# Optimization experiments

Measured on AMD Instinct MI355X. Metric: run time of the kernel, lower is better.

The kernel has to match this reference:

```python
import jax, jax.numpy as jnp
import numpy as np

NUM_HEADS = 12


def setup_inputs() -> dict:
    key = jax.random.key(0)
    ks = jax.random.split(key, 10)
    B, N, C = 8, 1024, 768
    H = NUM_HEADS
    return {
        "x": jax.random.normal(ks[0], (B, N, C), dtype=jnp.float32),
        "geometric": jax.random.uniform(ks[1], (B, 1, 1, 1), dtype=jnp.float32),
        "text": jax.random.uniform(ks[2], (B, 1, 1, 1), dtype=jnp.float32),
        "color": jax.random.uniform(ks[3], (B, 1, 1, 1), dtype=jnp.float32),
        "W_qkv": jax.random.normal(ks[4], (C, 3 * C), dtype=jnp.float32) * 0.02,
        "W_proj": jax.random.normal(ks[5], (C, C), dtype=jnp.float32) * 0.02,
        "b_proj": jax.random.normal(ks[6], (C,), dtype=jnp.float32) * 0.02,
        "geo_bias": jax.random.normal(ks[7], (1, H, 1, 1), dtype=jnp.float32) * 0.1,
        "txt_bias": jax.random.normal(ks[8], (1, H, 1, 1), dtype=jnp.float32) * 0.1,
        "col_bias": jax.random.normal(ks[9], (1, H, 1, 1), dtype=jnp.float32) * 0.1,
    }


def reference(x, geometric, text, color, W_qkv, W_proj, b_proj, geo_bias, txt_bias, col_bias):
    B, N, C = x.shape
    H = NUM_HEADS
    Dh = C // H
    scale = Dh ** -0.5
    # qkv: [B, N, 3, H, Dh] -> q,k,v each [B, H, N, Dh]
    qkv = (x @ W_qkv).reshape(B, N, 3, H, Dh)
    q = jnp.transpose(qkv[:, :, 0], (0, 2, 1, 3))
    k = jnp.transpose(qkv[:, :, 1], (0, 2, 1, 3))
    v = jnp.transpose(qkv[:, :, 2], (0, 2, 1, 3))
    # scores [B, H, N, N] with additive per-head logo biases
    attn = jnp.einsum("bhnd,bhmd->bhnm", q, k) * scale
    attn = attn + geo_bias * geometric + txt_bias * text + col_bias * color
    attn = jax.nn.softmax(attn, axis=-1)
    out = jnp.einsum("bhnm,bhmd->bhnd", attn, v)  # [B, H, N, Dh]
    out = jnp.transpose(out, (0, 2, 1, 3)).reshape(B, N, C)
    return out @ W_proj + b_proj
```

## Files before the change

kernel.cpp:

```cpp
#include <hip/hip_runtime.h>
#include <hip/hip_bf16.h>


typedef __bf16 b16x8 __attribute__((ext_vector_type(8)));
typedef float f32x4 __attribute__((ext_vector_type(4)));

__device__ __forceinline__ ushort f2b(float f) {
    union { float f; uint u; } v; v.f = f;
    uint u = v.u;
    u += 0x7fffu + ((u >> 16) & 1u);
    return (ushort)(u >> 16);
}

__device__ __forceinline__ uint packbf(float a, float b) {
    union { float f; uint u; } ua, ub; ua.f = a; ub.f = b;
    return ((ua.u + 0x8000u) >> 16) | ((ub.u + 0x8000u) & 0xffff0000u);
}

__device__ __forceinline__ void async_cp16(const void* g, void* l) {
    __builtin_amdgcn_global_load_lds(
        (const __attribute__((address_space(1))) unsigned int*)g,
        (__attribute__((address_space(3))) unsigned int*)l, 16, 0, 0);
}


__global__ __launch_bounds__(256)
void k_prep(const float* __restrict__ x, ushort* __restrict__ xb,
            const float* __restrict__ Wqkv, ushort* __restrict__ wqkvt,
            const float* __restrict__ Wproj, ushort* __restrict__ wprojt) {
    __shared__ ushort T[64][65];
    const int blk = blockIdx.x;
    const int t   = threadIdx.x;

    if (blk < 6144) {
        const int i = blk * 256 + t;
        const float4 v = reinterpret_cast<const float4*>(x)[i];
        ushort4 o;
        o.x = f2b(v.x); o.y = f2b(v.y); o.z = f2b(v.z); o.w = f2b(v.w);
        reinterpret_cast<ushort4*>(xb)[i] = o;
        return;
    }

    const bool isqkv = (blk < 6576);
    const int idx = isqkv ? (blk - 6144) : (blk - 6576);
    const int Nin = isqkv ? 2304 : 768;
    const float* W  = isqkv ? Wqkv : Wproj;
    ushort* Wt      = isqkv ? wqkvt : wprojt;
    const int k0 = (idx % 12) * 64;
    const int n0 = (idx / 12) * 64;
    const int r  = t >> 4, cg = (t & 15) * 4;
    #pragma unroll
    for (int rr = 0; rr < 64; rr += 16) {
        const float4 v = *reinterpret_cast<const float4*>(&W[(size_t)(k0 + r + rr) * Nin + n0 + cg]);
        T[r + rr][cg + 0] = f2b(v.x); T[r + rr][cg + 1] = f2b(v.y);
        T[r + rr][cg + 2] = f2b(v.z); T[r + rr][cg + 3] = f2b(v.w);
    }
    __syncthreads();
    #pragma unroll
    for (int rr = 0; rr < 64; rr += 16) {
        ushort4 o;
        o.x = T[cg + 0][r + rr]; o.y = T[cg + 1][r + rr];
        o.z = T[cg + 2][r + rr]; o.w = T[cg + 3][r + rr];
        *reinterpret_cast<ushort4*>(&Wt[(size_t)(n0 + r + rr) * 768 + k0 + cg]) = o;
    }
}


#define SBAR()   asm volatile("s_barrier" ::: "memory")
#define WAITV3() asm volatile("s_waitcnt vmcnt(3)" ::: "memory")
#define WAITV0() asm volatile("s_waitcnt vmcnt(0)" ::: "memory")

#define LDSA(buf, kh, ii) (*reinterpret_cast<const b16x8*>( \
    &lds[(buf) * 16384 + (kh) * 8192 + (wm * 64 + (ii) * 16 + m16) * 32 + q8s]))
#define LDSB(buf, kh, jj) (*reinterpret_cast<const b16x8*>( \
    &lds[32768 + (buf) * 8192 + (kh) * 4096 + (wn * 64 + (jj) * 16 + m16) * 32 + q8s]))

#define STA(bufn, ktv, kh) { \
    async_cp16(aA0 + (ktv) + (kh) * 32, &lds[(bufn)*16384 + (kh)*8192 + tid*8]); \
    async_cp16(aA1 + (ktv) + (kh) * 32, &lds[(bufn)*16384 + (kh)*8192 + 4096 + tid*8]); }
#define STB(bufn, ktv, kh) { \
    async_cp16(aB0 + (ktv) + (kh) * 32, &lds[32768 + (bufn)*8192 + (kh)*4096 + tid*8]); }

#define MPAIR(I0, kh, bufc) { \
    const b16x8 a0 = LDSA(bufc, kh, (I0)+0), a1 = LDSA(bufc, kh, (I0)+1); \
    if (vblk) { \
        _Pragma("unroll") \
        for (int j = 0; j < 4; j++) { \
            acc[(I0)+0][j] = __builtin_amdgcn_mfma_f32_16x16x32_bf16(a0, bf[j], acc[(I0)+0][j], 0, 0, 0); \
            acc[(I0)+1][j] = __builtin_amdgcn_mfma_f32_16x16x32_bf16(a1, bf[j], acc[(I0)+1][j], 0, 0, 0); \
        } \
    } else { \
        _Pragma("unroll") \
        for (int j = 0; j < 4; j++) { \
            acc[(I0)+0][j] = __builtin_amdgcn_mfma_f32_16x16x32_bf16(bf[j], a0, acc[(I0)+0][j], 0, 0, 0); \
            acc[(I0)+1][j] = __builtin_amdgcn_mfma_f32_16x16x32_bf16(bf[j], a1, acc[(I0)+1][j], 0, 0, 0); \
        } \
    } }

__global__ __launch_bounds__(512, 1)
void k_qkv(const ushort* __restrict__ A, const ushort* __restrict__ Bt,
           ushort* __restrict__ qo, ushort* __restrict__ ko,
           ushort* __restrict__ vo) {
    extern __shared__ ushort lds[];
    const int id   = blockIdx.x;
    const int xcd  = id & 7;
    const int s    = id >> 3;
    const int by   = xcd * 4 + s / 18;
    const int bx   = s % 18;
    const int tid  = threadIdx.x;
    const int w    = tid >> 6;
    const int lane = tid & 63;
    const int wm   = w >> 1, wn = w & 1;
    const int m16  = lane & 15, quad = lane >> 4;
    const int q8   = quad * 8;
    const int q8s  = q8 ^ ((m16 & 8) ? 16 : 0);
    const int mbase = by * 256, nbase = bx * 128;
    const int colbase = nbase + wn * 64;
    const bool vblk = (nbase >= 1536);
    const int tr   = tid >> 2;
    const int ssub = ((tid & 3) * 8) ^ ((tr & 8) ? 16 : 0);

    const ushort* aA0 = &A [(size_t)(mbase +       tr) * 768 + ssub];
    const ushort* aA1 = &A [(size_t)(mbase + 128 + tr) * 768 + ssub];
    const ushort* aB0 = &Bt[(size_t)(nbase +       tr) * 768 + ssub];

    f32x4 acc[4][4];
    #pragma unroll
    for (int i = 0; i < 4; i++)
        #pragma unroll
        for (int j = 0; j < 4; j++) acc[i][j] = (f32x4){0.f, 0.f, 0.f, 0.f};

    STA(0, 0, 0); STB(0, 0, 0);
    STA(0, 0, 1); STB(0, 0, 1);
    WAITV3();
    SBAR();

    b16x8 bf[4];
    int cur = 0;
    for (int t = 0; t < 12; t++) {
        const int kt  = t * 64;
        const int nxt = cur ^ 1;
        const bool more = (t < 11);
        #pragma unroll
        for (int j = 0; j < 4; j++) bf[j] = LDSB(cur, 0, j);
        if (more) STA(nxt, kt + 64, 0);
        __builtin_amdgcn_s_setprio(1);
        MPAIR(0, 0, cur);
        __builtin_amdgcn_s_setprio(0);
        SBAR();
        if (more) STB(nxt, kt + 64, 0);
        __builtin_amdgcn_s_setprio(1);
        MPAIR(2, 0, cur);
        __builtin_amdgcn_s_setprio(0);
        if (more) { WAITV3(); } else { WAITV0(); }
        SBAR();
        #pragma unroll
        for (int j = 0; j < 4; j++) bf[j] = LDSB(cur, 1, j);
        if (more) STA(nxt, kt + 64, 1);
        __builtin_amdgcn_s_setprio(1);
        MPAIR(0, 1, cur);
        __builtin_amdgcn_s_setprio(0);
        SBAR();
        if (more) STB(nxt, kt + 64, 1);
        __builtin_amdgcn_s_setprio(1);
        MPAIR(2, 1, cur);
        __builtin_amdgcn_s_setprio(0);
        if (more) {
            WAITV3();
            SBAR();
        }
        cur = nxt;
    }

    if (vblk) {
        #pragma unroll
        for (int j = 0; j < 4; j++) {
            const int rem = colbase + j * 16 + m16 - 1536;
            const int h = rem >> 6, d0 = rem & 63;
            #pragma unroll
            for (int i = 0; i < 4; i++) {
                const int tok0 = mbase + wm * 64 + i * 16 + quad * 4;
                const int b = tok0 >> 10, n0 = tok0 & 1023;
                ushort4 pk;
                pk.x = f2b(acc[i][j][0]); pk.y = f2b(acc[i][j][1]);
                pk.z = f2b(acc[i][j][2]); pk.w = f2b(acc[i][j][3]);
                *reinterpret_cast<ushort4*>(
                    &vo[((size_t)(b * 12 + h) * 64 + d0) * 1024 + n0]) = pk;
            }
        }
    } else {
        ushort* base  = (nbase >= 768) ? ko : qo;
        const int off = (nbase >= 768) ? 768 : 0;
        #pragma unroll
        for (int j = 0; j < 4; j++) {
            const int f0 = colbase + j * 16 + quad * 4 - off;
            const int h = f0 >> 6, d0 = f0 & 63;
            #pragma unroll
            for (int i = 0; i < 4; i++) {
                const int tok = mbase + wm * 64 + i * 16 + m16;
                const int b = tok >> 10, n = tok & 1023;
                ushort4 pk;
                pk.x = f2b(acc[i][j][0]); pk.y = f2b(acc[i][j][1]);
                pk.z = f2b(acc[i][j][2]); pk.w = f2b(acc[i][j][3]);
                *reinterpret_cast<ushort4*>(
                    &base[((size_t)(b * 12 + h) * 1024 + n) * 64 + d0]) = pk;
            }
        }
    }
}


__global__ __launch_bounds__(256, 2)
void k_proj(const ushort* __restrict__ A, const ushort* __restrict__ Bt,
            float* __restrict__ co, const float* __restrict__ bias,
            int N, int K) {
    __shared__ ushort As[2][128 * 32];
    __shared__ ushort Bs[2][128 * 32];
    const int id   = blockIdx.x;
    const int xcd  = id & 7;
    const int s    = id >> 3;
    const int by   = xcd * 8 + (s & 7);
    const int bx   = s >> 3;
    const int tid  = threadIdx.x;
    const int lane = tid & 63;
    const int w    = tid >> 6;
    const int wm   = w >> 1, wn = w & 1;
    const int m16  = lane & 15, quad = lane >> 4;
    const int mbase = by * 128, nbase = bx * 128;

    f32x4 acc[4][4];
    #pragma unroll
    for (int i = 0; i < 4; i++)
        #pragma unroll
        for (int j = 0; j < 4; j++) acc[i][j] = (f32x4){0.f, 0.f, 0.f, 0.f};

    const int rS = w * 32 + (lane >> 2);
    const int cS = (lane & 3) * 8;
    const int wOff0 = (w * 2 + 0) * 512;
    const int wOff1 = (w * 2 + 1) * 512;
    const ushort* gA0 = &A [(size_t)(mbase + rS)      * K + cS];
    const ushort* gA1 = &A [(size_t)(mbase + rS + 16) * K + cS];
    const ushort* gB0 = &Bt[(size_t)(nbase + rS)      * K + cS];
    const ushort* gB1 = &Bt[(size_t)(nbase + rS + 16) * K + cS];

    async_cp16(gA0, &As[0][wOff0]);
    async_cp16(gA1, &As[0][wOff1]);
    async_cp16(gB0, &Bs[0][wOff0]);
    async_cp16(gB1, &Bs[0][wOff1]);

    for (int kt = 0; kt < K; kt += 32) {
        const int cur = (kt >> 5) & 1, nxt = cur ^ 1;
        __syncthreads();
        if (kt + 32 < K) {
            async_cp16(gA0 + kt + 32, &As[nxt][wOff0]);
            async_cp16(gA1 + kt + 32, &As[nxt][wOff1]);
            async_cp16(gB0 + kt + 32, &Bs[nxt][wOff0]);
            async_cp16(gB1 + kt + 32, &Bs[nxt][wOff1]);
        }
        b16x8 af[4], bfr[4];
        #pragma unroll
        for (int i = 0; i < 4; i++)
            af[i] = *reinterpret_cast<const b16x8*>(&As[cur][(wm * 64 + i * 16 + m16) * 32 + quad * 8]);
        #pragma unroll
        for (int j = 0; j < 4; j++)
            bfr[j] = *reinterpret_cast<const b16x8*>(&Bs[cur][(wn * 64 + j * 16 + m16) * 32 + quad * 8]);
        #pragma unroll
        for (int i = 0; i < 4; i++)
            #pragma unroll
            for (int j = 0; j < 4; j++)
                acc[i][j] = __builtin_amdgcn_mfma_f32_16x16x32_bf16(bfr[j], af[i], acc[i][j], 0, 0, 0);
    }

    #pragma unroll
    for (int j = 0; j < 4; j++) {
        const int f0 = nbase + wn * 64 + j * 16 + quad * 4;
        #pragma unroll
        for (int i = 0; i < 4; i++) {
            const int tok = mbase + wm * 64 + i * 16 + m16;
            float4 val;
            val.x = acc[i][j][0] + bias[f0 + 0];
            val.y = acc[i][j][1] + bias[f0 + 1];
            val.z = acc[i][j][2] + bias[f0 + 2];
            val.w = acc[i][j][3] + bias[f0 + 3];
            *reinterpret_cast<float4*>(&co[(size_t)tok * N + f0]) = val;
        }
    }
}


#define AP 72

__global__ __launch_bounds__(256)
void k_attn(const ushort* __restrict__ qa, const ushort* __restrict__ ka,
            const ushort* __restrict__ vt, ushort* __restrict__ ao) {
    __shared__ ushort Ks[64 * AP];
    __shared__ ushort Vs[64 * AP];

    const int l    = blockIdx.x;
    const int xcd  = l & 7;
    const int g    = l >> 3;
    const int head = (g % 12) * 8 + xcd;
    const int qsup = g / 12;
    const int tid  = threadIdx.x;
    const int w    = tid >> 6;
    const int lane = tid & 63;
    const int n    = lane & 15;
    const int q    = lane >> 4;

    const ushort* qh = qa + (size_t)head * 65536;
    const ushort* kh = ka + (size_t)head * 65536;
    const ushort* vh = vt + (size_t)head * 65536;
    const int qrow0 = qsup * 128 + w * 32;

    b16x8 bq0[2], bq1[2];
    #pragma unroll
    for (int u = 0; u < 2; u++) {
        bq0[u] = *reinterpret_cast<const b16x8*>(&qh[(qrow0 + u * 16 + n) * 64 + q * 8]);
        bq1[u] = *reinterpret_cast<const b16x8*>(&qh[(qrow0 + u * 16 + n) * 64 + 32 + q * 8]);
    }

    const int kr0 = tid >> 3, kc0 = (tid & 7) * 8;
    const int kr1 = kr0 + 32, kc1 = kc0;

    int4 kg0, kg1, vg0, vg1;
    kg0 = *reinterpret_cast<const int4*>(&kh[(0 + kr0) * 64 + kc0]);
    kg1 = *reinterpret_cast<const int4*>(&kh[(0 + kr1) * 64 + kc1]);
    vg0 = *reinterpret_cast<const int4*>(&vh[kr0 * 1024 + 0 + kc0]);
    vg1 = *reinterpret_cast<const int4*>(&vh[kr1 * 1024 + 0 + kc1]);

    f32x4 o[2][4];
    #pragma unroll
    for (int u = 0; u < 2; u++)
        #pragma unroll
        for (int dt = 0; dt < 4; dt++) o[u][dt] = (f32x4){0, 0, 0, 0};
    float Lacc[2] = {0.f, 0.f};

    const float SC = 0.125f * 1.4426950408889634f;
    const int s0 = ((q & 1) * 2) * 16 + n;
    const int s1 = s0 + 16;
    const bool lowq = (q < 2);

    for (int m0 = 0; m0 < 1024; m0 += 64) {
        *reinterpret_cast<int4*>(&Ks[kr0 * AP + kc0]) = kg0;
        *reinterpret_cast<int4*>(&Ks[kr1 * AP + kc1]) = kg1;
        *reinterpret_cast<int4*>(&Vs[kr0 * AP + kc0]) = vg0;
        *reinterpret_cast<int4*>(&Vs[kr1 * AP + kc1]) = vg1;
        __syncthreads();

        if (m0 + 64 < 1024) {
            kg0 = *reinterpret_cast<const int4*>(&kh[(m0 + 64 + kr0) * 64 + kc0]);
            kg1 = *reinterpret_cast<const int4*>(&kh[(m0 + 64 + kr1) * 64 + kc1]);
            vg0 = *reinterpret_cast<const int4*>(&vh[kr0 * 1024 + m0 + 64 + kc0]);
            vg1 = *reinterpret_cast<const int4*>(&vh[kr1 * 1024 + m0 + 64 + kc1]);
        }

        #pragma unroll
        for (int mc = 0; mc < 2; mc++) {
            b16x8 ka0t[2], ka1t[2];
            #pragma unroll
            for (int t = 0; t < 2; t++) {
                ka0t[t] = *reinterpret_cast<const b16x8*>(&Ks[(mc * 32 + t * 16 + n) * AP + q * 8]);
                ka1t[t] = *reinterpret_cast<const b16x8*>(&Ks[(mc * 32 + t * 16 + n) * AP + 32 + q * 8]);
            }
            f32x4 st[2][2];
            #pragma unroll
            for (int u = 0; u < 2; u++)
                #pragma unroll
                for (int t = 0; t < 2; t++) {
                    st[u][t] = (f32x4){0, 0, 0, 0};
                    st[u][t] = __builtin_amdgcn_mfma_f32_16x16x32_bf16(ka0t[t], bq0[u], st[u][t], 0, 0, 0);
                    st[u][t] = __builtin_amdgcn_mfma_f32_16x16x32_bf16(ka1t[t], bq1[u], st[u][t], 0, 0, 0);
                }

            union { uint4 u4; b16x8 v; } bp[2];
            #pragma unroll
            for (int u = 0; u < 2; u++) {
                float p00 = __builtin_amdgcn_exp2f(st[u][0][0] * SC);
                float p01 = __builtin_amdgcn_exp2f(st[u][0][1] * SC);
                float p02 = __builtin_amdgcn_exp2f(st[u][0][2] * SC);
                float p03 = __builtin_amdgcn_exp2f(st[u][0][3] * SC);
                float p10 = __builtin_amdgcn_exp2f(st[u][1][0] * SC);
                float p11 = __builtin_amdgcn_exp2f(st[u][1][1] * SC);
                float p12 = __builtin_amdgcn_exp2f(st[u][1][2] * SC);
                float p13 = __builtin_amdgcn_exp2f(st[u][1][3] * SC);
                Lacc[u] += ((p00 + p01) + (p02 + p03)) + ((p10 + p11) + (p12 + p13));

                const uint pk00 = packbf(p00, p01), pk01 = packbf(p02, p03);
                const uint pk10 = packbf(p10, p11), pk11 = packbf(p12, p13);

                uint a, b, dw0, dw1, dw2, dw3;
                a = __shfl((int)pk00, s0); b = __shfl((int)pk10, s0); dw0 = lowq ? a : b;
                a = __shfl((int)pk01, s0); b = __shfl((int)pk11, s0); dw1 = lowq ? a : b;
                a = __shfl((int)pk00, s1); b = __shfl((int)pk10, s1); dw2 = lowq ? a : b;
                a = __shfl((int)pk01, s1); b = __shfl((int)pk11, s1); dw3 = lowq ? a : b;
                bp[u].u4 = (uint4){dw0, dw1, dw2, dw3};
            }

            #pragma unroll
            for (int dt = 0; dt < 4; dt++) {
                const b16x8 av = *reinterpret_cast<const b16x8*>(
                    &Vs[(dt * 16 + n) * AP + mc * 32 + q * 8]);
                #pragma unroll
                for (int u = 0; u < 2; u++)
                    o[u][dt] = __builtin_amdgcn_mfma_f32_16x16x32_bf16(av, bp[u].v, o[u][dt], 0, 0, 0);
            }
        }
        __syncthreads();
    }

    const int bb = head / 12, h = head - bb * 12;
    #pragma unroll
    for (int u = 0; u < 2; u++) {
        float L = Lacc[u];
        L += __shfl_xor(L, 16);
        L += __shfl_xor(L, 32);
        const float inv = 1.f / L;
        ushort* dst = ao + ((size_t)(bb * 1024 + qrow0 + u * 16 + n)) * 768 + h * 64 + q * 4;
        #pragma unroll
        for (int dt = 0; dt < 4; dt++) {
            ushort4 pk;
            pk.x = f2b(o[u][dt][0] * inv);
            pk.y = f2b(o[u][dt][1] * inv);
            pk.z = f2b(o[u][dt][2] * inv);
            pk.w = f2b(o[u][dt][3] * inv);
            *reinterpret_cast<ushort4*>(dst + dt * 16) = pk;
        }
    }
}


extern "C" void kernel_launch(void* const* d_in, const int* in_sizes, int n_in,
                              void* d_out, int out_size, void* d_ws, size_t ws_size,
                              hipStream_t stream) {
    (void)in_sizes; (void)n_in; (void)out_size; (void)ws_size;
    const float* x     = (const float*)d_in[0];
    const float* Wqkv  = (const float*)d_in[4];
    const float* Wproj = (const float*)d_in[5];
    const float* bproj = (const float*)d_in[6];
    float* out = (float*)d_out;

    char* ws = (char*)d_ws;
    ushort* xb     = (ushort*)ws; ws += (size_t)8192 * 768 * 2;
    ushort* wqkvt  = (ushort*)ws; ws += (size_t)2304 * 768 * 2;
    ushort* wprojt = (ushort*)ws; ws += (size_t)768  * 768 * 2;
    ushort* qa     = (ushort*)ws; ws += (size_t)96 * 1024 * 64 * 2;
    ushort* ka     = (ushort*)ws; ws += (size_t)96 * 1024 * 64 * 2;
    ushort* vt     = (ushort*)ws; ws += (size_t)96 * 64 * 1024 * 2;
    ushort* ao     = (ushort*)ws; ws += (size_t)8192 * 768 * 2;

    static int attr_set = 0;
    if (!attr_set) {
        hipFuncSetAttribute((const void*)k_qkv,
                            hipFuncAttributeMaxDynamicSharedMemorySize, 98304);
        attr_set = 1;
    }

    k_prep<<<dim3(6720), dim3(256), 0, stream>>>(x, xb, Wqkv, wqkvt, Wproj, wprojt);
    k_qkv<<<dim3(576), dim3(512), 98304, stream>>>(xb, wqkvt, qa, ka, vt);
    k_attn<<<dim3(768), dim3(256), 0, stream>>>(qa, ka, vt, ao);
    k_proj<<<dim3(384), dim3(256), 0, stream>>>(ao, wprojt, out, bproj, 768, 768);
}
```

Measured before the change: 224.2 us.

## Restructure QKV GEMM into 3-slot ring of 32-wide k stages

Replaces the double-buffered 64-wide k pipeline with a three-slot ring buffer of 32-wide k stages. Each iteration issues one combined A+B async stage two steps ahead and needs a single barrier, where the old loop used four. LDS use drops from 96 KB dynamic to 72 KB static, and the min-blocks hint is removed from launch bounds. The aim is fewer barriers and deeper prefetch; the cost is smaller per-stage work, which may expose more latency.

Measured after the change: 227.5 us. About the same (+1.5%).

```diff
diff --git a/kernel.cpp b/kernel.cpp
--- a/kernel.cpp
+++ b/kernel.cpp
@@ -70,19 +70,18 @@
 #define WAITV3() asm volatile("s_waitcnt vmcnt(3)" ::: "memory")
 #define WAITV0() asm volatile("s_waitcnt vmcnt(0)" ::: "memory")
 
-#define LDSA(buf, kh, ii) (*reinterpret_cast<const b16x8*>( \
-    &lds[(buf) * 16384 + (kh) * 8192 + (wm * 64 + (ii) * 16 + m16) * 32 + q8s]))
-#define LDSB(buf, kh, jj) (*reinterpret_cast<const b16x8*>( \
-    &lds[32768 + (buf) * 8192 + (kh) * 4096 + (wn * 64 + (jj) * 16 + m16) * 32 + q8s]))
-
-#define STA(bufn, ktv, kh) { \
-    async_cp16(aA0 + (ktv) + (kh) * 32, &lds[(bufn)*16384 + (kh)*8192 + tid*8]); \
-    async_cp16(aA1 + (ktv) + (kh) * 32, &lds[(bufn)*16384 + (kh)*8192 + 4096 + tid*8]); }
-#define STB(bufn, ktv, kh) { \
-    async_cp16(aB0 + (ktv) + (kh) * 32, &lds[32768 + (bufn)*8192 + (kh)*4096 + tid*8]); }
-
-#define MPAIR(I0, kh, bufc) { \
-    const b16x8 a0 = LDSA(bufc, kh, (I0)+0), a1 = LDSA(bufc, kh, (I0)+1); \
+#define LDSA(slot, ii) (*reinterpret_cast<const b16x8*>( \
+    &lds[(slot) * 8192 + (wm * 64 + (ii) * 16 + m16) * 32 + q8s]))
+#define LDSB(slot, jj) (*reinterpret_cast<const b16x8*>( \
+    &lds[24576 + (slot) * 4096 + (wn * 64 + (jj) * 16 + m16) * 32 + q8s]))
+
+#define STAGE(slot, colOff) { \
+    async_cp16(aA0 + (colOff), &lds[(slot) * 8192 + tid * 8]); \
+    async_cp16(aA1 + (colOff), &lds[(slot) * 8192 + 4096 + tid * 8]); \
+    async_cp16(aB0 + (colOff), &lds[24576 + (slot) * 4096 + tid * 8]); }
+
+#define MPAIR(I0, slot) { \
+    const b16x8 a0 = LDSA(slot, (I0)+0), a1 = LDSA(slot, (I0)+1); \
     if (vblk) { \
         _Pragma("unroll") \
         for (int j = 0; j < 4; j++) { \
@@ -97,11 +96,11 @@
         } \
     } }
 
-__global__ __launch_bounds__(512, 1)
+__global__ __launch_bounds__(512)
 void k_qkv(const ushort* __restrict__ A, const ushort* __restrict__ Bt,
            ushort* __restrict__ qo, ushort* __restrict__ ko,
            ushort* __restrict__ vo) {
-    extern __shared__ ushort lds[];
+    __shared__ ushort lds[36864];
     const int id   = blockIdx.x;
     const int xcd  = id & 7;
     const int s    = id >> 3;
@@ -130,46 +129,25 @@
         #pragma unroll
         for (int j = 0; j < 4; j++) acc[i][j] = (f32x4){0.f, 0.f, 0.f, 0.f};
 
-    STA(0, 0, 0); STB(0, 0, 0);
-    STA(0, 0, 1); STB(0, 0, 1);
+    STAGE(0, 0);
+    STAGE(1, 32);
     WAITV3();
     SBAR();
 
     b16x8 bf[4];
     int cur = 0;
-    for (int t = 0; t < 12; t++) {
-        const int kt  = t * 64;
-        const int nxt = cur ^ 1;
-        const bool more = (t < 11);
-        #pragma unroll
-        for (int j = 0; j < 4; j++) bf[j] = LDSB(cur, 0, j);
-        if (more) STA(nxt, kt + 64, 0);
+    for (int h = 0; h < 24; ++h) {
+        const int stageSlot = (cur == 0) ? 2 : cur - 1;
+        #pragma unroll
+        for (int j = 0; j < 4; j++) bf[j] = LDSB(cur, j);
+        if (h < 22) STAGE(stageSlot, (h + 2) * 32);
         __builtin_amdgcn_s_setprio(1);
-        MPAIR(0, 0, cur);
+        MPAIR(0, cur);
+        MPAIR(2, cur);
         __builtin_amdgcn_s_setprio(0);
-        SBAR();
-        if (more) STB(nxt, kt + 64, 0);
-        __builtin_amdgcn_s_setprio(1);
-        MPAIR(2, 0, cur);
-        __builtin_amdgcn_s_setprio(0);
-        if (more) { WAITV3(); } else { WAITV0(); }
-        SBAR();
-        #pragma unroll
-        for (int j = 0; j < 4; j++) bf[j] = LDSB(cur, 1, j);
-        if (more) STA(nxt, kt + 64, 1);
-        __builtin_amdgcn_s_setprio(1);
-        MPAIR(0, 1, cur);
-        __builtin_amdgcn_s_setprio(0);
-        SBAR();
-        if (more) STB(nxt, kt + 64, 1);
-        __builtin_amdgcn_s_setprio(1);
-        MPAIR(2, 1, cur);
-        __builtin_amdgcn_s_setprio(0);
-        if (more) {
-            WAITV3();
-            SBAR();
-        }
-        cur = nxt;
+        if (h < 22) { WAITV3(); } else { WAITV0(); }
+        if (h < 23) SBAR();
+        cur = (cur == 2) ? 0 : cur + 1;
     }
 
     if (vblk) {
@@ -448,15 +426,8 @@
     ushort* vt     = (ushort*)ws; ws += (size_t)96 * 64 * 1024 * 2;
     ushort* ao     = (ushort*)ws; ws += (size_t)8192 * 768 * 2;
 
-    static int attr_set = 0;
-    if (!attr_set) {
-        hipFuncSetAttribute((const void*)k_qkv,
-                            hipFuncAttributeMaxDynamicSharedMemorySize, 98304);
-        attr_set = 1;
-    }
-
     k_prep<<<dim3(6720), dim3(256), 0, stream>>>(x, xb, Wqkv, wqkvt, Wproj, wprojt);
-    k_qkv<<<dim3(576), dim3(512), 98304, stream>>>(xb, wqkvt, qa, ka, vt);
+    k_qkv<<<dim3(576), dim3(512), 0, stream>>>(xb, wqkvt, qa, ka, vt);
     k_attn<<<dim3(768), dim3(256), 0, stream>>>(qa, ka, vt, ao);
     k_proj<<<dim3(384), dim3(256), 0, stream>>>(ao, wprojt, out, bproj, 768, 768);
 }
```
